# Kernel optimization log

Hardware: AMD Instinct MI355X
Metric: run time of the kernel (lower is better)

The kernel has to match this reference:

```python
import jax, jax.numpy as jnp
import numpy as np

DIM = 1024
H = 16
DH = DIM // H
K = 4
B = 8
N = 2048
EPS = 1e-6


def _depthwise_conv_silu(x, w, n):
    # x: (B, N, C), w: (C, 1, K)  -- torch Conv1d depthwise, padding=K//2, truncate to n, SiLU
    pad = K // 2
    y = jax.lax.conv_general_dilated(
        x.transpose(0, 2, 1), w, window_strides=(1,), padding=[(pad, pad)],
        dimension_numbers=('NCH', 'OIH', 'NCH'), feature_group_count=x.shape[-1])
    y = y[..., :n]  # for even K the conv output is n+1; torch truncates
    return jax.nn.silu(y).transpose(0, 2, 1)


def _l2norm(x):
    return x / (jnp.linalg.norm(x, axis=-1, keepdims=True) + EPS)


def setup_inputs() -> dict:
    key = jax.random.key(0)
    ks = jax.random.split(key, 16)
    s = 1.0 / np.sqrt(DIM)
    d = dict(
        x=jax.random.normal(ks[0], (B, N, DIM), jnp.float32),
        Wq=jax.random.normal(ks[1], (DIM, DIM), jnp.float32) * s,
        bq=jnp.zeros((DIM,), jnp.float32),
        Wk=jax.random.normal(ks[2], (DIM, DIM), jnp.float32) * s,
        bk=jnp.zeros((DIM,), jnp.float32),
        Wv=jax.random.normal(ks[3], (DIM, DIM), jnp.float32) * s,
        bv=jnp.zeros((DIM,), jnp.float32),
        Wa=jax.random.normal(ks[4], (H, DIM), jnp.float32) * s,
        ba=jnp.zeros((H,), jnp.float32),
        Wb=jax.random.normal(ks[5], (H, DIM), jnp.float32) * s,
        bb=jnp.zeros((H,), jnp.float32),
        conv_q=jax.random.normal(ks[6], (DIM, 1, K), jnp.float32) * 0.5,
        conv_k=jax.random.normal(ks[7], (DIM, 1, K), jnp.float32) * 0.5,
        conv_v=jax.random.normal(ks[8], (DIM, 1, K), jnp.float32) * 0.5,
        Wo=jax.random.normal(ks[9], (DIM, DIM), jnp.float32) * s,
        bo=jnp.zeros((DIM,), jnp.float32),
    )
    return d


def _forward(x, Wq, bq, Wk, bk, Wv, bv, Wa, ba, Wb, bb, conv_q, conv_k, conv_v, Wo, bo):
    b_, n_, c_ = x.shape
    q = _l2norm(_depthwise_conv_silu(jax.nn.silu(x @ Wq.T + bq), conv_q, n_))
    k = _l2norm(_depthwise_conv_silu(jax.nn.silu(x @ Wk.T + bk), conv_k, n_))
    v = _depthwise_conv_silu(jax.nn.silu(x @ Wv.T + bv), conv_v, n_)
    a = jax.nn.sigmoid(x @ Wa.T + ba)  # (B, N, H)
    bgate = jax.nn.sigmoid(x @ Wb.T + bb)  # (B, N, H)

    # (N, B, H, Dh) for scan over time
    q = q.reshape(b_, n_, H, DH).transpose(1, 0, 2, 3)
    k = k.reshape(b_, n_, H, DH).transpose(1, 0, 2, 3)
    v = v.reshape(b_, n_, H, DH).transpose(1, 0, 2, 3)
    a = a.transpose(1, 0, 2)
    bgate = bgate.transpose(1, 0, 2)

    S0 = jnp.zeros((b_, H, DH, DH), x.dtype)

    def step(S, inp):
        qt, kt, vt, at, bt = inp  # qt/kt/vt: (B,H,Dh), at/bt: (B,H)
        at = at[..., None, None]
        bt = bt[..., None, None]
        # S_new = S @ (a*(I - b k k^T)) + b * v k^T
        #       = a*S - a*b*(S k) k^T + b * v k^T
        Sk = jnp.einsum('bhde,bhe->bhd', S, kt)
        outer_Sk_k = Sk[..., :, None] * kt[..., None, :]
        outer_v_k = vt[..., :, None] * kt[..., None, :]
        S_new = at * S - at * bt * outer_Sk_k + bt * outer_v_k
        # o_e = sum_d q_d S[d, e]
        ot = jnp.einsum('bhd,bhde->bhe', qt, S_new)
        return S_new, ot

    _, O = jax.lax.scan(step, S0, (q, k, v, a, bgate))  # O: (N, B, H, Dh)
    O = O.transpose(1, 0, 2, 3).reshape(b_, n_, c_)
    return O @ Wo.T + bo


def reference(x, Wq, bq, Wk, bk, Wv, bv, Wa, ba, Wb, bb, conv_q, conv_k, conv_v, Wo, bo):
    return _forward(x, Wq, bq, Wk, bk, Wv, bv, Wa, ba, Wb, bb, conv_q, conv_k, conv_v, Wo, bo)
```

## Files before the change

kernel.cpp:

```cpp
#include <hip/hip_runtime.h>

#define DIMC 1024
#define SEQ  2048
#define NHEAD 16
#define BATCH 8

__device__ __forceinline__ void gll4(const float* g, float* l) {
  __builtin_amdgcn_global_load_lds(
      (const __attribute__((address_space(1))) void*)g,
      (__attribute__((address_space(3))) void*)l, 4, 0, 0);
}
__device__ __forceinline__ void gll16(const unsigned short* g, unsigned short* l) {
  __builtin_amdgcn_global_load_lds(
      (const __attribute__((address_space(1))) void*)g,
      (__attribute__((address_space(3))) void*)l, 16, 0, 0);
}

#define WAIT_VM42   0x8F7A
#define WAIT_VM0    0x0F70

__device__ __forceinline__ unsigned short f2bf(float f) {
  unsigned u = __float_as_uint(f);
  return (unsigned short)((u + 0x7fffu + ((u >> 16) & 1u)) >> 16);
}
__device__ __forceinline__ float bf2f(unsigned short h) {
  return __uint_as_float(((unsigned)h) << 16);
}

typedef __attribute__((ext_vector_type(8))) short  bf16x8;
typedef __attribute__((ext_vector_type(4))) float  floatx4;

__device__ __forceinline__ float oct_sum(float x) {
  int t1 = __builtin_amdgcn_update_dpp(0, __float_as_int(x), 0xB1, 0xF, 0xF, true);
  float x1 = x + __int_as_float(t1);
  int t2 = __builtin_amdgcn_update_dpp(0, __float_as_int(x1), 0x4E, 0xF, 0xF, true);
  float x2 = x1 + __int_as_float(t2);
  int t3 = __builtin_amdgcn_update_dpp(0, __float_as_int(x2), 0x141, 0xF, 0xF, true);
  return x2 + __int_as_float(t3);
}

__global__ __launch_bounds__(256)
void cvt_split(const float* __restrict__ in, unsigned short* __restrict__ hi,
               unsigned short* __restrict__ lo, int n4)
{
  int i = blockIdx.x * 256 + threadIdx.x;
  if (i >= n4) return;
  float4 f = ((const float4*)in)[i];
  unsigned short h0 = f2bf(f.x), h1 = f2bf(f.y), h2 = f2bf(f.z), h3 = f2bf(f.w);
  unsigned short l0 = f2bf(f.x - bf2f(h0)), l1 = f2bf(f.y - bf2f(h1));
  unsigned short l2 = f2bf(f.z - bf2f(h2)), l3 = f2bf(f.w - bf2f(h3));
  ushort4 H; H.x = h0; H.y = h1; H.z = h2; H.w = h3;
  ushort4 L; L.x = l0; L.y = l1; L.z = l2; L.w = l3;
  ((ushort4*)hi)[i] = H;
  ((ushort4*)lo)[i] = L;
}

__global__ void pack_ab_kernel(const float* __restrict__ Wa, const float* __restrict__ ba,
                               const float* __restrict__ Wb, const float* __restrict__ bb,
                               float* __restrict__ Wab, float* __restrict__ bab)
{
  int i = blockIdx.x * 256 + threadIdx.x;
  if (i < 128 * 1024) {
    int row = i >> 10, col = i & 1023;
    float v = 0.0f;
    if (row < 16) v = Wa[(row << 10) + col];
    else if (row < 32) v = Wb[((row - 16) << 10) + col];
    Wab[i] = v;
  } else {
    int j = i - 128 * 1024;
    if (j < 128) {
      float v = 0.0f;
      if (j < 16) v = ba[j];
      else if (j < 32) v = bb[j - 16];
      bab[j] = v;
    }
  }
}

__global__ __launch_bounds__(256, 2)
void gemm_bf16x3(const unsigned short* __restrict__ Ah, const unsigned short* __restrict__ Al,
                 const unsigned short* __restrict__ Bh, const unsigned short* __restrict__ Bl,
                 const float* __restrict__ bias, float* __restrict__ C,
                 int K, int ldc, int nvalid, int act)
{
  __shared__ unsigned short sAh[4096], sAl[4096], sBh[4096], sBl[4096];
  const int tid  = threadIdx.x;
  const int lane = tid & 63;
  const int w    = tid >> 6;

  const int crow = tid >> 2;
  const int kel  = (tid & 3) << 3;
  const unsigned short* pAh0 = Ah + (size_t)(blockIdx.x * 128 + crow) * K + kel;
  const unsigned short* pAh1 = Ah + (size_t)(blockIdx.x * 128 + 64 + crow) * K + kel;
  const unsigned short* pAl0 = Al + (size_t)(blockIdx.x * 128 + crow) * K + kel;
  const unsigned short* pAl1 = Al + (size_t)(blockIdx.x * 128 + 64 + crow) * K + kel;
  const unsigned short* pBh0 = Bh + (size_t)(blockIdx.y * 128 + crow) * K + kel;
  const unsigned short* pBh1 = Bh + (size_t)(blockIdx.y * 128 + 64 + crow) * K + kel;
  const unsigned short* pBl0 = Bl + (size_t)(blockIdx.y * 128 + crow) * K + kel;
  const unsigned short* pBl1 = Bl + (size_t)(blockIdx.y * 128 + 64 + crow) * K + kel;
  const int wb = (tid & 192) * 8;

  floatx4 acc[16];
  #pragma unroll
  for (int i = 0; i < 16; ++i) acc[i] = (floatx4){0.f, 0.f, 0.f, 0.f};

  const int mq = (w & 1) << 6;
  const int nq = (w >> 1) << 6;
  const int fr = lane & 15;
  const int fk = (lane >> 4) << 3;

  for (int kt = 0; kt < K; kt += 32) {
    __syncthreads();
    gll16(pAh0, sAh + wb); gll16(pAh1, sAh + 2048 + wb);
    gll16(pAl0, sAl + wb); gll16(pAl1, sAl + 2048 + wb);
    gll16(pBh0, sBh + wb); gll16(pBh1, sBh + 2048 + wb);
    gll16(pBl0, sBl + wb); gll16(pBl1, sBl + 2048 + wb);
    pAh0 += 32; pAh1 += 32; pAl0 += 32; pAl1 += 32;
    pBh0 += 32; pBh1 += 32; pBl0 += 32; pBl1 += 32;
    __syncthreads();

    bf16x8 ah[4], al[4], bh[4], bl[4];
    #pragma unroll
    for (int mi = 0; mi < 4; ++mi) {
      int off = (mq + mi * 16 + fr) * 32 + fk;
      ah[mi] = *(const bf16x8*)&sAh[off];
      al[mi] = *(const bf16x8*)&sAl[off];
    }
    #pragma unroll
    for (int ni = 0; ni < 4; ++ni) {
      int off = (nq + ni * 16 + fr) * 32 + fk;
      bh[ni] = *(const bf16x8*)&sBh[off];
      bl[ni] = *(const bf16x8*)&sBl[off];
    }
    #pragma unroll
    for (int mi = 0; mi < 4; ++mi)
      #pragma unroll
      for (int ni = 0; ni < 4; ++ni) {
        floatx4 c = acc[mi * 4 + ni];
        c = __builtin_amdgcn_mfma_f32_16x16x32_bf16(ah[mi], bh[ni], c, 0, 0, 0);
        c = __builtin_amdgcn_mfma_f32_16x16x32_bf16(ah[mi], bl[ni], c, 0, 0, 0);
        c = __builtin_amdgcn_mfma_f32_16x16x32_bf16(al[mi], bh[ni], c, 0, 0, 0);
        acc[mi * 4 + ni] = c;
      }
  }

  const int mbase = blockIdx.x * 128 + mq + ((lane >> 4) << 2);
  const int nbase = blockIdx.y * 128 + nq + (lane & 15);
  #pragma unroll
  for (int ni = 0; ni < 4; ++ni) {
    int n = nbase + ni * 16;
    if (n < nvalid) {
      float bs = bias[n];
      #pragma unroll
      for (int mi = 0; mi < 4; ++mi) {
        #pragma unroll
        for (int r = 0; r < 4; ++r) {
          int m = mbase + mi * 16 + r;
          float val = acc[mi * 4 + ni][r] + bs;
          if (act == 1)      val = val * (1.0f / (1.0f + __expf(-val)));
          else if (act == 2) val = 1.0f / (1.0f + __expf(-val));
          C[(size_t)m * ldc + n] = val;
        }
      }
    }
  }
}

__global__ __launch_bounds__(256)
void conv_kernel(const float* __restrict__ pre, const float* __restrict__ w,
                 float* __restrict__ out, int do_norm)
{
  __shared__ float red[4];
  const int bt  = blockIdx.x;
  const int t   = bt & (SEQ - 1);
  const int tid = threadIdx.x;
  const int c   = tid << 2;
  const float* rowp = pre + (size_t)bt * DIMC + c;
  const float4 z = make_float4(0.f, 0.f, 0.f, 0.f);
  float4 xm2 = (t >= 2)      ? *(const float4*)(rowp - 2 * DIMC) : z;
  float4 xm1 = (t >= 1)      ? *(const float4*)(rowp - DIMC)     : z;
  float4 x0  =                 *(const float4*)(rowp);
  float4 xp1 = (t + 1 < SEQ) ? *(const float4*)(rowp + DIMC)     : z;
  const float4 w0 = *(const float4*)(w + (size_t)(c + 0) * 4);
  const float4 w1 = *(const float4*)(w + (size_t)(c + 1) * 4);
  const float4 w2 = *(const float4*)(w + (size_t)(c + 2) * 4);
  const float4 w3 = *(const float4*)(w + (size_t)(c + 3) * 4);
  float y0 = xm2.x * w0.x + xm1.x * w0.y + x0.x * w0.z + xp1.x * w0.w;
  float y1 = xm2.y * w1.x + xm1.y * w1.y + x0.y * w1.z + xp1.y * w1.w;
  float y2 = xm2.z * w2.x + xm1.z * w2.y + x0.z * w2.z + xp1.z * w2.w;
  float y3 = xm2.w * w3.x + xm1.w * w3.y + x0.w * w3.z + xp1.w * w3.w;
  y0 = y0 * (1.0f / (1.0f + __expf(-y0)));
  y1 = y1 * (1.0f / (1.0f + __expf(-y1)));
  y2 = y2 * (1.0f / (1.0f + __expf(-y2)));
  y3 = y3 * (1.0f / (1.0f + __expf(-y3)));
  if (do_norm) {
    float ss = y0*y0 + y1*y1 + y2*y2 + y3*y3;
    #pragma unroll
    for (int off = 32; off >= 1; off >>= 1) ss += __shfl_xor(ss, off);
    if ((tid & 63) == 0) red[tid >> 6] = ss;
    __syncthreads();
    float tot = red[0] + red[1] + red[2] + red[3];
    float rn = 1.0f / (sqrtf(tot) + 1e-6f);
    y0 *= rn; y1 *= rn; y2 *= rn; y3 *= rn;
  }
  *(float4*)(out + (size_t)bt * DIMC + c) = make_float4(y0, y1, y2, y3);
}

#define PD 16
__global__ __launch_bounds__(64)
void scan2_kernel(const float* __restrict__ k, const float* __restrict__ v,
                  const float* __restrict__ ab, float* __restrict__ Cf,
                  float* __restrict__ SC)
{
  __shared__ float ring[PD][2][64];
  __shared__ float aS[SEQ];
  __shared__ float bSh[SEQ];
  const int blk = blockIdx.x;
  const int bh  = blk >> 3;
  const int dg  = blk & 7;
  const int b   = bh >> 4, h = bh & 15;
  const int tid = threadIdx.x;
  const int eh  = tid & 7;
  const int d   = dg * 8 + (tid >> 3);
  const int e0  = eh * 8;

  const float* abbase = ab + (size_t)b * SEQ * 32 + h;
  for (int i = tid; i < SEQ; i += 64) {
    aS[i]  = abbase[(size_t)i * 32];
    bSh[i] = abbase[(size_t)i * 32 + 16];
  }

  const size_t base = (size_t)b * SEQ * DIMC + h * 64;
  const float* kp = k + base + tid;
  const float* vp = v + base + tid;

  {
    float4 z4 = make_float4(0.f, 0.f, 0.f, 0.f);
    float4* dst0 = (float4*)&SC[(((size_t)bh * 32) * 64 + d) * 64 + e0];
    dst0[0] = z4; dst0[1] = z4;
  }

  #pragma unroll
  for (int pt = 0; pt < PD; ++pt) {
    gll4(kp + (size_t)pt * DIMC, &ring[pt][0][0]);
    gll4(vp + (size_t)pt * DIMC, &ring[pt][1][0]);
  }
  __builtin_amdgcn_s_waitcnt(WAIT_VM0);
  asm volatile("" ::: "memory");

  float S[8];
  #pragma unroll
  for (int j = 0; j < 8; ++j) S[j] = 0.f;

  float* cfp = Cf + (size_t)bh * SEQ * 64 + d;

  float4 k1a = *(const float4*)&ring[0][0][e0];
  float4 k1b = *(const float4*)&ring[0][0][e0 + 4];
  float4 k2a = *(const float4*)&ring[1][0][e0];
  float4 k2b = *(const float4*)&ring[1][0][e0 + 4];
  float  v1  = ring[0][1][d];
  float  v2  = ring[1][1][d];
  float  a1  = aS[0], a2 = aS[1];
  float  b1  = bSh[0], b2 = bSh[1];

  for (int t = 0; t < SEQ; t += 2) {
    float q0 = fmaf(S[0], k1a.x, S[4] * k1b.x);
    float q1 = fmaf(S[1], k1a.y, S[5] * k1b.y);
    float q2 = fmaf(S[2], k1a.z, S[6] * k1b.z);
    float q3 = fmaf(S[3], k1a.w, S[7] * k1b.w);
    float r0 = fmaf(S[0], k2a.x, S[4] * k2b.x);
    float r1 = fmaf(S[1], k2a.y, S[5] * k2b.y);
    float r2 = fmaf(S[2], k2a.z, S[6] * k2b.z);
    float r3 = fmaf(S[3], k2a.w, S[7] * k2b.w);
    float x0 = fmaf(k1a.x, k2a.x, k1b.x * k2b.x);
    float x1 = fmaf(k1a.y, k2a.y, k1b.y * k2b.y);
    float x2 = fmaf(k1a.z, k2a.z, k1b.z * k2b.z);
    float x3 = fmaf(k1a.w, k2a.w, k1b.w * k2b.w);
    float u1  = oct_sum((q0 + q1) + (q2 + q3));
    float u2  = oct_sum((r0 + r1) + (r2 + r3));
    float kap = oct_sum((x0 + x1) + (x2 + x3));

    const float e1 = b1 * v1, f1 = a1 * b1;
    const float e2 = b2 * v2, f2 = a2 * b2;
    const float w2 = a1 * u2;
    const float G2 = a1 * a2;
    const float c1 = fmaf(-f1, u1, e1);
    const float c2 = fmaf(-f2, fmaf(c1, kap, w2), e2);
    const float d1 = a2 * c1;
    if (eh == 0) { cfp[(size_t)t * 64] = c1; cfp[(size_t)(t + 1) * 64] = c2; }
    asm volatile("" ::: "memory");

    if (t < SEQ - PD) {
      const int s0 = t & (PD - 1);
      const int s1 = (t + 1) & (PD - 1);
      gll4(kp + (size_t)(t + PD) * DIMC,     &ring[s0][0][0]);
      gll4(vp + (size_t)(t + PD) * DIMC,     &ring[s0][1][0]);
      gll4(kp + (size_t)(t + PD + 1) * DIMC, &ring[s1][0][0]);
      gll4(vp + (size_t)(t + PD + 1) * DIMC, &ring[s1][1][0]);
      asm volatile("" ::: "memory");
      __builtin_amdgcn_s_waitcnt(WAIT_VM42);
    } else {
      asm volatile("" ::: "memory");
      __builtin_amdgcn_s_waitcnt(WAIT_VM0);
    }
    asm volatile("" ::: "memory");

    const int sl2 = (t + 2) & (PD - 1);
    const int sl3 = (t + 3) & (PD - 1);
    const int tn  = (t + 2) & (SEQ - 1);
    const float4 k1a_n = *(const float4*)&ring[sl2][0][e0];
    const float4 k1b_n = *(const float4*)&ring[sl2][0][e0 + 4];
    const float4 k2a_n = *(const float4*)&ring[sl3][0][e0];
    const float4 k2b_n = *(const float4*)&ring[sl3][0][e0 + 4];
    const float  v1_n  = ring[sl2][1][d];
    const float  v2_n  = ring[sl3][1][d];
    const float2 a_n   = *(const float2*)&aS[tn];
    const float2 b_n   = *(const float2*)&bSh[tn];

    S[0] = fmaf(G2, S[0], fmaf(d1, k1a.x, c2 * k2a.x));
    S[1] = fmaf(G2, S[1], fmaf(d1, k1a.y, c2 * k2a.y));
    S[2] = fmaf(G2, S[2], fmaf(d1, k1a.z, c2 * k2a.z));
    S[3] = fmaf(G2, S[3], fmaf(d1, k1a.w, c2 * k2a.w));
    S[4] = fmaf(G2, S[4], fmaf(d1, k1b.x, c2 * k2b.x));
    S[5] = fmaf(G2, S[5], fmaf(d1, k1b.y, c2 * k2b.y));
    S[6] = fmaf(G2, S[6], fmaf(d1, k1b.z, c2 * k2b.z));
    S[7] = fmaf(G2, S[7], fmaf(d1, k1b.w, c2 * k2b.w));

    if (((t + 2) & 63) == 0 && (t + 2) < SEQ) {
      float4* dst = (float4*)&SC[(((size_t)bh * 32 + ((t + 2) >> 6)) * 64 + d) * 64 + e0];
      dst[0] = make_float4(S[0], S[1], S[2], S[3]);
      dst[1] = make_float4(S[4], S[5], S[6], S[7]);
    }

    k1a = k1a_n; k1b = k1b_n; k2a = k2a_n; k2b = k2b_n;
    v1 = v1_n; v2 = v2_n; a1 = a_n.x; a2 = a_n.y; b1 = b_n.x; b2 = b_n.y;
  }
}

__global__ __launch_bounds__(256)
void outp_kernel(const float* __restrict__ q, const float* __restrict__ k,
                 const float* __restrict__ Cf, const float* __restrict__ SC,
                 const float* __restrict__ ab, float* __restrict__ O)
{
  __shared__ float QsT[64 * 64];
  __shared__ float CP [64 * 64];
  __shared__ float Ks [64 * 64];
  __shared__ float Zs [64 * 64];
  __shared__ float av[64], Gv[64], rGv[64];

  const int c   = blockIdx.x;
  const int bh  = blockIdx.y;
  const int b   = bh >> 4, h = bh & 15;
  const int cs  = c << 6;
  const int tid = threadIdx.x;
  const int tl  = tid & 63, th = tid >> 6;

  {
    const float* qr = q  + ((size_t)(b * SEQ + cs + tl)) * DIMC + h * 64 + th * 16;
    const float* cr = Cf + ((size_t)bh * SEQ + cs + tl) * 64 + th * 16;
    #pragma unroll
    for (int u = 0; u < 4; ++u) {
      float4 qv = *(const float4*)(qr + u * 4);
      float4 cv = *(const float4*)(cr + u * 4);
      int dd = th * 16 + u * 4;
      QsT[(dd+0)*64 + tl] = qv.x; QsT[(dd+1)*64 + tl] = qv.y;
      QsT[(dd+2)*64 + tl] = qv.z; QsT[(dd+3)*64 + tl] = qv.w;
      CP [(dd+0)*64 + tl] = cv.x; CP [(dd+1)*64 + tl] = cv.y;
      CP [(dd+2)*64 + tl] = cv.z; CP [(dd+3)*64 + tl] = cv.w;
    }
    const float* kr = k  + ((size_t)(b * SEQ + cs + tl)) * DIMC + h * 64 + th * 16;
    const float* zr = SC + (((size_t)bh * 32 + c) * 64 + tl) * 64 + th * 16;
    #pragma unroll
    for (int u = 0; u < 4; ++u) {
      *(float4*)&Ks[tl * 64 + th * 16 + u * 4] = *(const float4*)(kr + u * 4);
      *(float4*)&Zs[tl * 64 + th * 16 + u * 4] = *(const float4*)(zr + u * 4);
    }
    if (tid < 64) av[tid] = ab[((size_t)(b * SEQ + cs + tid)) * 32 + h];
  }
  __syncthreads();
  if (tid == 0) {
    float g = 1.f;
    for (int t = 0; t < 64; ++t) { g *= av[t]; Gv[t] = fmaxf(g, 1e-37f); }
  }
  __syncthreads();
  if (tid < 64) rGv[tid] = 1.0f / Gv[tid];
  __syncthreads();

  const int tq = (tid >> 4) << 2;
  const int s0 = (tid & 15) << 2;

  float p[4][4] = {{0.f}};
  #pragma unroll 4
  for (int dd = 0; dd < 64; ++dd) {
    const float4 qv = *(const float4*)&QsT[dd * 64 + tq];
    const float4 cv = *(const float4*)&CP [dd * 64 + s0];
    const float qa[4] = {qv.x, qv.y, qv.z, qv.w};
    const float ca[4] = {cv.x, cv.y, cv.z, cv.w};
    #pragma unroll
    for (int i = 0; i < 4; ++i)
      #pragma unroll
      for (int j = 0; j < 4; ++j)
        p[i][j] = fmaf(qa[i], ca[j], p[i][j]);
  }
  __syncthreads();

  #pragma unroll
  for (int i = 0; i < 4; ++i) {
    const float gt = Gv[tq + i];
    #pragma unroll
    for (int j = 0; j < 4; ++j) {
      float vsc = (s0 + j <= tq + i) ? p[i][j] * gt * rGv[s0 + j] : 0.f;
      CP[(s0 + j) * 64 + (tq + i)] = vsc;
    }
  }
  __syncthreads();

  const int e0 = s0;
  float o[4][4] = {{0.f}};
  #pragma unroll 4
  for (int ss = 0; ss < 64; ++ss) {
    const float4 pv = *(const float4*)&CP[ss * 64 + tq];
    const float4 kv = *(const float4*)&Ks[ss * 64 + e0];
    const float pa[4] = {pv.x, pv.y, pv.z, pv.w};
    const float ka[4] = {kv.x, kv.y, kv.z, kv.w};
    #pragma unroll
    for (int i = 0; i < 4; ++i)
      #pragma unroll
      for (int j = 0; j < 4; ++j)
        o[i][j] = fmaf(pa[i], ka[j], o[i][j]);
  }
  float zt[4][4] = {{0.f}};
  #pragma unroll 4
  for (int dd = 0; dd < 64; ++dd) {
    const float4 qv = *(const float4*)&QsT[dd * 64 + tq];
    const float4 zv = *(const float4*)&Zs[dd * 64 + e0];
    const float qa[4] = {qv.x, qv.y, qv.z, qv.w};
    const float za[4] = {zv.x, zv.y, zv.z, zv.w};
    #pragma unroll
    for (int i = 0; i < 4; ++i)
      #pragma unroll
      for (int j = 0; j < 4; ++j)
        zt[i][j] = fmaf(qa[i], za[j], zt[i][j]);
  }
  #pragma unroll
  for (int i = 0; i < 4; ++i) {
    const float gt = Gv[tq + i];
    float4 res;
    res.x = fmaf(gt, zt[i][0], o[i][0]);
    res.y = fmaf(gt, zt[i][1], o[i][1]);
    res.z = fmaf(gt, zt[i][2], o[i][2]);
    res.w = fmaf(gt, zt[i][3], o[i][3]);
    *(float4*)(O + ((size_t)(b * SEQ + cs + tq + i)) * DIMC + h * 64 + e0) = res;
  }
}

extern "C" void kernel_launch(void* const* d_in, const int* in_sizes, int n_in,
                              void* d_out, int out_size, void* d_ws, size_t ws_size,
                              hipStream_t stream)
{
  const float* x  = (const float*)d_in[0];
  const float* Wq = (const float*)d_in[1];
  const float* bq = (const float*)d_in[2];
  const float* Wk = (const float*)d_in[3];
  const float* bk = (const float*)d_in[4];
  const float* Wv = (const float*)d_in[5];
  const float* bv = (const float*)d_in[6];
  const float* Wa = (const float*)d_in[7];
  const float* ba = (const float*)d_in[8];
  const float* Wb = (const float*)d_in[9];
  const float* bb = (const float*)d_in[10];
  const float* cq = (const float*)d_in[11];
  const float* ck = (const float*)d_in[12];
  const float* cv = (const float*)d_in[13];
  const float* Wo = (const float*)d_in[14];
  const float* bo = (const float*)d_in[15];
  float* out = (float*)d_out;
  float* ws  = (float*)d_ws;

  const size_t per_b = (size_t)SEQ * DIMC;
  const size_t wsz   = (size_t)DIMC * DIMC;

  int bc = BATCH;
  while (bc > 1) {
    size_t fl = 4 * (size_t)bc * per_b + (size_t)bc * SEQ * 32 + 128 * 1024 + 128;
    size_t us = 2 * (size_t)bc * per_b + 8 * wsz + 2 * 128 * 1024;
    if (fl * 4 + us * 2 <= ws_size) break;
    bc >>= 1;
  }

  float* P   = ws;
  float* qb  = P  + (size_t)bc * per_b;
  float* kb  = qb + (size_t)bc * per_b;
  float* vb  = kb + (size_t)bc * per_b;
  float* abb = vb + (size_t)bc * per_b;
  float* Wab = abb + (size_t)bc * SEQ * 32;
  float* bab = Wab + 128 * 1024;
  unsigned short* xh   = (unsigned short*)(bab + 128);
  unsigned short* xl   = xh  + (size_t)bc * per_b;
  unsigned short* wqh  = xl  + (size_t)bc * per_b;
  unsigned short* wql  = wqh + wsz;
  unsigned short* wkh  = wql + wsz;
  unsigned short* wkl  = wkh + wsz;
  unsigned short* wvh  = wkl + wsz;
  unsigned short* wvl  = wvh + wsz;
  unsigned short* woh  = wvl + wsz;
  unsigned short* wol  = woh + wsz;
  unsigned short* wabh = wol + wsz;
  unsigned short* wabl = wabh + 128 * 1024;

  float* Cf  = (float*)xh;
  float* SCp = P;

  pack_ab_kernel<<<513, 256, 0, stream>>>(Wa, ba, Wb, bb, Wab, bab);
  cvt_split<<<(int)(wsz / 4 + 255) / 256, 256, 0, stream>>>(Wq, wqh, wql, (int)(wsz / 4));
  cvt_split<<<(int)(wsz / 4 + 255) / 256, 256, 0, stream>>>(Wk, wkh, wkl, (int)(wsz / 4));
  cvt_split<<<(int)(wsz / 4 + 255) / 256, 256, 0, stream>>>(Wv, wvh, wvl, (int)(wsz / 4));
  cvt_split<<<(int)(wsz / 4 + 255) / 256, 256, 0, stream>>>(Wo, woh, wol, (int)(wsz / 4));
  cvt_split<<<(128 * 1024 / 4 + 255) / 256, 256, 0, stream>>>(Wab, wabh, wabl, 128 * 1024 / 4);

  for (int b0 = 0; b0 < BATCH; b0 += bc) {
    const float* xb = x + (size_t)b0 * per_b;
    const int M = bc * SEQ;
    const int n4 = (int)((size_t)bc * per_b / 4);
    dim3 gg(M / 128, DIMC / 128);
    dim3 gab(M / 128, 1);

    cvt_split<<<(n4 + 255) / 256, 256, 0, stream>>>(xb, xh, xl, n4);

    gemm_bf16x3<<<gg, 256, 0, stream>>>(xh, xl, wqh, wql, bq, P, DIMC, DIMC, DIMC, 1);
    conv_kernel<<<dim3(M), 256, 0, stream>>>(P, cq, qb, 1);
    gemm_bf16x3<<<gg, 256, 0, stream>>>(xh, xl, wkh, wkl, bk, P, DIMC, DIMC, DIMC, 1);
    conv_kernel<<<dim3(M), 256, 0, stream>>>(P, ck, kb, 1);
    gemm_bf16x3<<<gg, 256, 0, stream>>>(xh, xl, wvh, wvl, bv, P, DIMC, DIMC, DIMC, 1);
    conv_kernel<<<dim3(M), 256, 0, stream>>>(P, cv, vb, 0);
    gemm_bf16x3<<<gab, 256, 0, stream>>>(xh, xl, wabh, wabl, bab, abb, DIMC, 32, 32, 2);
    scan2_kernel<<<dim3(bc * NHEAD * 8), 64, 0, stream>>>(kb, vb, abb, Cf, SCp);
    outp_kernel<<<dim3(SEQ / 64, bc * NHEAD), 256, 0, stream>>>(qb, kb, Cf, SCp, abb, vb);
    cvt_split<<<(n4 + 255) / 256, 256, 0, stream>>>(vb, xh, xl, n4);
    gemm_bf16x3<<<gg, 256, 0, stream>>>(xh, xl, woh, wol, bo, out + (size_t)b0 * per_b, DIMC, DIMC, DIMC, 0);
  }
}
```

Measured before the change: 1.620 ms.

## Store k and v per head in an interleaved layout for wide scan prefetch

The conv kernel now writes k and v into a per-(batch,head) interleaved buffer, [t][k 64 | v 64] per head, so the scan kernel can prefetch two timesteps with a single 16-byte global-to-LDS load per lane instead of four 4-byte loads. The scan now stages per-timestep coefficients in shared memory and writes them in chunk-major blocks once every 64 steps, replacing scattered per-step stores, and outp reads those blocks contiguously. The output projection now uses the final output buffer as its intermediate instead of vb. The change adds more complex indexing and shared-memory staging in the latency-bound serial scan loop.

Result: faster. 1.562 ms (-3.6%).

```diff
diff --git a/kernel.cpp b/kernel.cpp
--- a/kernel.cpp
+++ b/kernel.cpp
@@ -5,18 +5,18 @@
 #define NHEAD 16
 #define BATCH 8
 
-__device__ __forceinline__ void gll4(const float* g, float* l) {
-  __builtin_amdgcn_global_load_lds(
-      (const __attribute__((address_space(1))) void*)g,
-      (__attribute__((address_space(3))) void*)l, 4, 0, 0);
-}
-__device__ __forceinline__ void gll16(const unsigned short* g, unsigned short* l) {
+__device__ __forceinline__ void gll16u(const unsigned short* g, unsigned short* l) {
   __builtin_amdgcn_global_load_lds(
       (const __attribute__((address_space(1))) void*)g,
       (__attribute__((address_space(3))) void*)l, 16, 0, 0);
 }
-
-#define WAIT_VM42   0x8F7A
+__device__ __forceinline__ void gll16f(const float* g, float* l) {
+  __builtin_amdgcn_global_load_lds(
+      (const __attribute__((address_space(1))) void*)g,
+      (__attribute__((address_space(3))) void*)l, 16, 0, 0);
+}
+
+#define WAIT_VM7    0x0F77
 #define WAIT_VM0    0x0F70
 
 __device__ __forceinline__ unsigned short f2bf(float f) {
@@ -111,10 +111,10 @@
 
   for (int kt = 0; kt < K; kt += 32) {
     __syncthreads();
-    gll16(pAh0, sAh + wb); gll16(pAh1, sAh + 2048 + wb);
-    gll16(pAl0, sAl + wb); gll16(pAl1, sAl + 2048 + wb);
-    gll16(pBh0, sBh + wb); gll16(pBh1, sBh + 2048 + wb);
-    gll16(pBl0, sBl + wb); gll16(pBl1, sBl + 2048 + wb);
+    gll16u(pAh0, sAh + wb); gll16u(pAh1, sAh + 2048 + wb);
+    gll16u(pAl0, sAl + wb); gll16u(pAl1, sAl + 2048 + wb);
+    gll16u(pBh0, sBh + wb); gll16u(pBh1, sBh + 2048 + wb);
+    gll16u(pBl0, sBl + wb); gll16u(pBl1, sBl + 2048 + wb);
     pAh0 += 32; pAh1 += 32; pAl0 += 32; pAl1 += 32;
     pBh0 += 32; pBh1 += 32; pBl0 += 32; pBl1 += 32;
     __syncthreads();
@@ -168,7 +168,7 @@
 
 __global__ __launch_bounds__(256)
 void conv_kernel(const float* __restrict__ pre, const float* __restrict__ w,
-                 float* __restrict__ out, int do_norm)
+                 float* __restrict__ out, int do_norm, int mode)
 {
   __shared__ float red[4];
   const int bt  = blockIdx.x;
@@ -203,25 +203,33 @@
     float rn = 1.0f / (sqrtf(tot) + 1e-6f);
     y0 *= rn; y1 *= rn; y2 *= rn; y3 *= rn;
   }
-  *(float4*)(out + (size_t)bt * DIMC + c) = make_float4(y0, y1, y2, y3);
+  float4 res = make_float4(y0, y1, y2, y3);
+  if (mode == 0) {
+    *(float4*)(out + (size_t)bt * DIMC + c) = res;
+  } else {
+    const int b = bt >> 11;
+    const int h = c >> 6, e = c & 63;
+    const int koff = (mode == 1) ? 0 : 64;
+    *(float4*)(out + (((size_t)(b * 16 + h)) * SEQ + t) * 128 + koff + e) = res;
+  }
 }
 
 #define PD 16
 __global__ __launch_bounds__(64)
-void scan2_kernel(const float* __restrict__ k, const float* __restrict__ v,
-                  const float* __restrict__ ab, float* __restrict__ Cf,
-                  float* __restrict__ SC)
-{
-  __shared__ float ring[PD][2][64];
+void scan2_kernel(const float* __restrict__ kv, const float* __restrict__ ab,
+                  float* __restrict__ Cf, float* __restrict__ SC)
+{
+  __shared__ float ring[8][256];
   __shared__ float aS[SEQ];
   __shared__ float bSh[SEQ];
-  const int blk = blockIdx.x;
-  const int bh  = blk >> 3;
-  const int dg  = blk & 7;
+  __shared__ float cbuf[8][72];
+  const int bh  = blockIdx.x;
+  const int dg  = blockIdx.y;
   const int b   = bh >> 4, h = bh & 15;
   const int tid = threadIdx.x;
   const int eh  = tid & 7;
-  const int d   = dg * 8 + (tid >> 3);
+  const int dl  = tid >> 3;
+  const int d   = dg * 8 + dl;
   const int e0  = eh * 8;
 
   const float* abbase = ab + (size_t)b * SEQ * 32 + h;
@@ -230,9 +238,7 @@
     bSh[i] = abbase[(size_t)i * 32 + 16];
   }
 
-  const size_t base = (size_t)b * SEQ * DIMC + h * 64;
-  const float* kp = k + base + tid;
-  const float* vp = v + base + tid;
+  const float* kvsrc = kv + (size_t)bh * SEQ * 128 + tid * 4;
 
   {
     float4 z4 = make_float4(0.f, 0.f, 0.f, 0.f);
@@ -241,10 +247,8 @@
   }
 
   #pragma unroll
-  for (int pt = 0; pt < PD; ++pt) {
-    gll4(kp + (size_t)pt * DIMC, &ring[pt][0][0]);
-    gll4(vp + (size_t)pt * DIMC, &ring[pt][1][0]);
-  }
+  for (int pp = 0; pp < 8; ++pp)
+    gll16f(kvsrc + (size_t)pp * 256, &ring[pp][0]);
   __builtin_amdgcn_s_waitcnt(WAIT_VM0);
   asm volatile("" ::: "memory");
 
@@ -252,14 +256,12 @@
   #pragma unroll
   for (int j = 0; j < 8; ++j) S[j] = 0.f;
 
-  float* cfp = Cf + (size_t)bh * SEQ * 64 + d;
-
-  float4 k1a = *(const float4*)&ring[0][0][e0];
-  float4 k1b = *(const float4*)&ring[0][0][e0 + 4];
-  float4 k2a = *(const float4*)&ring[1][0][e0];
-  float4 k2b = *(const float4*)&ring[1][0][e0 + 4];
-  float  v1  = ring[0][1][d];
-  float  v2  = ring[1][1][d];
+  float4 k1a = *(const float4*)&ring[0][e0];
+  float4 k1b = *(const float4*)&ring[0][e0 + 4];
+  float  v1  = ring[0][64 + d];
+  float4 k2a = *(const float4*)&ring[0][128 + e0];
+  float4 k2b = *(const float4*)&ring[0][128 + e0 + 4];
+  float  v2  = ring[0][192 + d];
   float  a1  = aS[0], a2 = aS[1];
   float  b1  = bSh[0], b2 = bSh[1];
 
@@ -280,40 +282,38 @@
     float u2  = oct_sum((r0 + r1) + (r2 + r3));
     float kap = oct_sum((x0 + x1) + (x2 + x3));
 
-    const float e1 = b1 * v1, f1 = a1 * b1;
-    const float e2 = b2 * v2, f2 = a2 * b2;
-    const float w2 = a1 * u2;
-    const float G2 = a1 * a2;
-    const float c1 = fmaf(-f1, u1, e1);
-    const float c2 = fmaf(-f2, fmaf(c1, kap, w2), e2);
-    const float d1 = a2 * c1;
-    if (eh == 0) { cfp[(size_t)t * 64] = c1; cfp[(size_t)(t + 1) * 64] = c2; }
+    const float e1c = b1 * v1, f1 = a1 * b1;
+    const float e2c = b2 * v2, f2 = a2 * b2;
+    const float w2c = a1 * u2;
+    const float G2  = a1 * a2;
+    const float c1  = fmaf(-f1, u1, e1c);
+    const float c2  = fmaf(-f2, fmaf(c1, kap, w2c), e2c);
+    const float d1  = a2 * c1;
+    if (eh == 0) {
+      float2* cw = (float2*)&cbuf[dl][t & 63];
+      *cw = make_float2(c1, c2);
+    }
+
     asm volatile("" ::: "memory");
-
     if (t < SEQ - PD) {
-      const int s0 = t & (PD - 1);
-      const int s1 = (t + 1) & (PD - 1);
-      gll4(kp + (size_t)(t + PD) * DIMC,     &ring[s0][0][0]);
-      gll4(vp + (size_t)(t + PD) * DIMC,     &ring[s0][1][0]);
-      gll4(kp + (size_t)(t + PD + 1) * DIMC, &ring[s1][0][0]);
-      gll4(vp + (size_t)(t + PD + 1) * DIMC, &ring[s1][1][0]);
+      const int slot = (t >> 1) & 7;
+      gll16f(kvsrc + (size_t)(t + PD) * 128, &ring[slot][0]);
       asm volatile("" ::: "memory");
-      __builtin_amdgcn_s_waitcnt(WAIT_VM42);
+      __builtin_amdgcn_s_waitcnt(WAIT_VM7);
     } else {
       asm volatile("" ::: "memory");
       __builtin_amdgcn_s_waitcnt(WAIT_VM0);
     }
     asm volatile("" ::: "memory");
 
-    const int sl2 = (t + 2) & (PD - 1);
-    const int sl3 = (t + 3) & (PD - 1);
-    const int tn  = (t + 2) & (SEQ - 1);
-    const float4 k1a_n = *(const float4*)&ring[sl2][0][e0];
-    const float4 k1b_n = *(const float4*)&ring[sl2][0][e0 + 4];
-    const float4 k2a_n = *(const float4*)&ring[sl3][0][e0];
-    const float4 k2b_n = *(const float4*)&ring[sl3][0][e0 + 4];
-    const float  v1_n  = ring[sl2][1][d];
-    const float  v2_n  = ring[sl3][1][d];
+    const int sl = ((t >> 1) + 1) & 7;
+    const int tn = (t + 2) & (SEQ - 1);
+    const float4 k1a_n = *(const float4*)&ring[sl][e0];
+    const float4 k1b_n = *(const float4*)&ring[sl][e0 + 4];
+    const float  v1_n  = ring[sl][64 + d];
+    const float4 k2a_n = *(const float4*)&ring[sl][128 + e0];
+    const float4 k2b_n = *(const float4*)&ring[sl][128 + e0 + 4];
+    const float  v2_n  = ring[sl][192 + d];
     const float2 a_n   = *(const float2*)&aS[tn];
     const float2 b_n   = *(const float2*)&bSh[tn];
 
@@ -326,10 +326,20 @@
     S[6] = fmaf(G2, S[6], fmaf(d1, k1b.z, c2 * k2b.z));
     S[7] = fmaf(G2, S[7], fmaf(d1, k1b.w, c2 * k2b.w));
 
-    if (((t + 2) & 63) == 0 && (t + 2) < SEQ) {
-      float4* dst = (float4*)&SC[(((size_t)bh * 32 + ((t + 2) >> 6)) * 64 + d) * 64 + e0];
-      dst[0] = make_float4(S[0], S[1], S[2], S[3]);
-      dst[1] = make_float4(S[4], S[5], S[6], S[7]);
+    if (((t + 2) & 63) == 0) {
+      const int cix  = t >> 6;
+      const int d2l  = tid >> 3;
+      const int toff = (tid & 7) << 3;
+      float* dst = Cf + (((size_t)bh * 32 + cix) * 64 + dg * 8 + d2l) * 64 + toff;
+      float4 f0 = *(const float4*)&cbuf[d2l][toff];
+      float4 f1 = *(const float4*)&cbuf[d2l][toff + 4];
+      *(float4*)dst       = f0;
+      *(float4*)(dst + 4) = f1;
+      if ((t + 2) < SEQ) {
+        float4* ck = (float4*)&SC[(((size_t)bh * 32 + ((t + 2) >> 6)) * 64 + d) * 64 + e0];
+        ck[0] = make_float4(S[0], S[1], S[2], S[3]);
+        ck[1] = make_float4(S[4], S[5], S[6], S[7]);
+      }
     }
 
     k1a = k1a_n; k1b = k1b_n; k2a = k2a_n; k2b = k2b_n;
@@ -338,7 +348,7 @@
 }
 
 __global__ __launch_bounds__(256)
-void outp_kernel(const float* __restrict__ q, const float* __restrict__ k,
+void outp_kernel(const float* __restrict__ q, const float* __restrict__ kv,
                  const float* __restrict__ Cf, const float* __restrict__ SC,
                  const float* __restrict__ ab, float* __restrict__ O)
 {
@@ -356,19 +366,19 @@
   const int tl  = tid & 63, th = tid >> 6;
 
   {
-    const float* qr = q  + ((size_t)(b * SEQ + cs + tl)) * DIMC + h * 64 + th * 16;
-    const float* cr = Cf + ((size_t)bh * SEQ + cs + tl) * 64 + th * 16;
+    const float* qr = q + ((size_t)(b * SEQ + cs + tl)) * DIMC + h * 64 + th * 16;
     #pragma unroll
     for (int u = 0; u < 4; ++u) {
       float4 qv = *(const float4*)(qr + u * 4);
-      float4 cv = *(const float4*)(cr + u * 4);
       int dd = th * 16 + u * 4;
       QsT[(dd+0)*64 + tl] = qv.x; QsT[(dd+1)*64 + tl] = qv.y;
       QsT[(dd+2)*64 + tl] = qv.z; QsT[(dd+3)*64 + tl] = qv.w;
-      CP [(dd+0)*64 + tl] = cv.x; CP [(dd+1)*64 + tl] = cv.y;
-      CP [(dd+2)*64 + tl] = cv.z; CP [(dd+3)*64 + tl] = cv.w;
-    }
-    const float* kr = k  + ((size_t)(b * SEQ + cs + tl)) * DIMC + h * 64 + th * 16;
+    }
+    const float* cr = Cf + ((size_t)bh * 32 + c) * 4096;
+    #pragma unroll
+    for (int u = 0; u < 4; ++u)
+      *(float4*)&CP[tid * 16 + u * 4] = *(const float4*)(cr + tid * 16 + u * 4);
+    const float* kr = kv + ((size_t)bh * SEQ + cs + tl) * 128 + th * 16;
     const float* zr = SC + (((size_t)bh * 32 + c) * 64 + tl) * 64 + th * 16;
     #pragma unroll
     for (int u = 0; u < 4; ++u) {
@@ -420,9 +430,9 @@
   #pragma unroll 4
   for (int ss = 0; ss < 64; ++ss) {
     const float4 pv = *(const float4*)&CP[ss * 64 + tq];
-    const float4 kv = *(const float4*)&Ks[ss * 64 + e0];
+    const float4 kvv = *(const float4*)&Ks[ss * 64 + e0];
     const float pa[4] = {pv.x, pv.y, pv.z, pv.w};
-    const float ka[4] = {kv.x, kv.y, kv.z, kv.w};
+    const float ka[4] = {kvv.x, kvv.y, kvv.z, kvv.w};
     #pragma unroll
     for (int i = 0; i < 4; ++i)
       #pragma unroll
@@ -490,9 +500,8 @@
 
   float* P   = ws;
   float* qb  = P  + (size_t)bc * per_b;
-  float* kb  = qb + (size_t)bc * per_b;
-  float* vb  = kb + (size_t)bc * per_b;
-  float* abb = vb + (size_t)bc * per_b;
+  float* kvp = qb + (size_t)bc * per_b;
+  float* abb = kvp + 2 * (size_t)bc * per_b;
   float* Wab = abb + (size_t)bc * SEQ * 32;
   float* bab = Wab + 128 * 1024;
   unsigned short* xh   = (unsigned short*)(bab + 128);
@@ -520,23 +529,25 @@
 
   for (int b0 = 0; b0 < BATCH; b0 += bc) {
     const float* xb = x + (size_t)b0 * per_b;
+    float* outb = out + (size_t)b0 * per_b;
     const int M = bc * SEQ;
     const int n4 = (int)((size_t)bc * per_b / 4);
+    const int nbh = bc * NHEAD;
     dim3 gg(M / 128, DIMC / 128);
     dim3 gab(M / 128, 1);
 
     cvt_split<<<(n4 + 255) / 256, 256, 0, stream>>>(xb, xh, xl, n4);
 
     gemm_bf16x3<<<gg, 256, 0, stream>>>(xh, xl, wqh, wql, bq, P, DIMC, DIMC, DIMC, 1);
-    conv_kernel<<<dim3(M), 256, 0, stream>>>(P, cq, qb, 1);
+    conv_kernel<<<dim3(M), 256, 0, stream>>>(P, cq, qb, 1, 0);
     gemm_bf16x3<<<gg, 256, 0, stream>>>(xh, xl, wkh, wkl, bk, P, DIMC, DIMC, DIMC, 1);
-    conv_kernel<<<dim3(M), 256, 0, stream>>>(P, ck, kb, 1);
+    conv_kernel<<<dim3(M), 256, 0, stream>>>(P, ck, kvp, 1, 1);
     gemm_bf16x3<<<gg, 256, 0, stream>>>(xh, xl, wvh, wvl, bv, P, DIMC, DIMC, DIMC, 1);
-    conv_kernel<<<dim3(M), 256, 0, stream>>>(P, cv, vb, 0);
+    conv_kernel<<<dim3(M), 256, 0, stream>>>(P, cv, kvp, 0, 2);
     gemm_bf16x3<<<gab, 256, 0, stream>>>(xh, xl, wabh, wabl, bab, abb, DIMC, 32, 32, 2);
-    scan2_kernel<<<dim3(bc * NHEAD * 8), 64, 0, stream>>>(kb, vb, abb, Cf, SCp);
-    outp_kernel<<<dim3(SEQ / 64, bc * NHEAD), 256, 0, stream>>>(qb, kb, Cf, SCp, abb, vb);
-    cvt_split<<<(n4 + 255) / 256, 256, 0, stream>>>(vb, xh, xl, n4);
-    gemm_bf16x3<<<gg, 256, 0, stream>>>(xh, xl, woh, wol, bo, out + (size_t)b0 * per_b, DIMC, DIMC, DIMC, 0);
-  }
-}
+    scan2_kernel<<<dim3(nbh, 8), 64, 0, stream>>>(kvp, abb, Cf, SCp);
+    outp_kernel<<<dim3(SEQ / 64, nbh), 256, 0, stream>>>(qb, kvp, Cf, SCp, abb, outb);
+    cvt_split<<<(n4 + 255) / 256, 256, 0, stream>>>(outb, xh, xl, n4);
+    gemm_bf16x3<<<gg, 256, 0, stream>>>(xh, xl, woh, wol, bo, outb, DIMC, DIMC, DIMC, 0);
+  }
+}
```
